# Optimization experiments

Hardware: AMD Instinct MI355X
Metric: run time of the kernel (lower is better)

The kernel has to match this reference:

```python
import jax, jax.numpy as jnp
import numpy as np

D_IN, D, BOX, REL, THR = 2048, 512, 8, 80, 0.5

def _ln(x, g, b):
    m = jnp.mean(x, -1, keepdims=True)
    v = jnp.mean((x - m) ** 2, -1, keepdims=True)
    return (x - m) * jax.lax.rsqrt(v + 1e-5) * g + b

def setup_inputs():
    key = jax.random.key(0)
    ks = jax.random.split(key, 24)
    B, N = 32, 50
    def lin(k, i, o):
        return jax.random.normal(k, (i, o), jnp.float32) / np.sqrt(i)
    z = lambda n: jnp.zeros((n,), jnp.float32)
    o = lambda n: jnp.ones((n,), jnp.float32)
    return {
        "images": jax.random.normal(ks[0], (B, N, D_IN), jnp.float32),
        "selfbbox": jax.random.uniform(ks[1], (B, N, BOX), jnp.float32),
        "bbox": jax.random.uniform(ks[2], (B, N, N, BOX), jnp.float32),
        "pre_w": lin(ks[3], D_IN, D), "pre_b": z(D), "pre_g": o(D), "pre_be": z(D),
        "subj_w": lin(ks[4], D, D), "subj_b": z(D),
        "obj_w": lin(ks[5], D, D), "obj_b": z(D),
        "ps1_w": lin(ks[6], BOX, 64), "ps1_b": z(64), "ps_g": o(64), "ps_be": z(64),
        "ps2_w": lin(ks[7], 64, 64), "ps2_b": z(64),
        "pr1_w": lin(ks[8], BOX, 64), "pr1_b": z(64), "pr_g": o(64), "pr_be": z(64),
        "pr2_w": lin(ks[9], 64, 64), "pr2_b": z(64),
        "rs_w": lin(ks[10], D + 64, 1), "rs_b": z(1),
        "rf_w": lin(ks[11], D + 64, REL), "rf_b": z(REL),
        "g1_w": lin(ks[12], D + REL, D + REL), "g1_b": z(D + REL),
        "g2_w": lin(ks[13], D + REL, D), "g2_b": z(D),
        "g3_w": lin(ks[14], D, D), "g3_b": z(D),
    }

def reference(images, selfbbox, bbox, pre_w, pre_b, pre_g, pre_be, subj_w, subj_b,
              obj_w, obj_b, ps1_w, ps1_b, ps_g, ps_be, ps2_w, ps2_b,
              pr1_w, pr1_b, pr_g, pr_be, pr2_w, pr2_b, rs_w, rs_b, rf_w, rf_b,
              g1_w, g1_b, g2_w, g2_b, g3_w, g3_b):
    B, N = images.shape[0], images.shape[1]
    mask = jnp.sum(images, -1) != 0.0                      # [B,N] valid nodes
    attention_mask = (~mask)[:, None, None, :]             # [B,1,1,N]
    mf = mask.astype(images.dtype)
    # preprocess: Linear -> ReLU -> (dropout=id at eval) -> LayerNorm
    x = _ln(jax.nn.relu(images @ pre_w + pre_b), pre_g, pre_be)  # [B,N,512]
    x_subj = jax.nn.relu(x @ subj_w + subj_b) * mf[..., None]
    x_obj = jax.nn.relu(x @ obj_w + obj_b) * mf[..., None]
    eye = jnp.eye(N, dtype=bool)
    # pairwise subject/object features: diag(i==j) holds subject, off-diag object j
    x_rela = jnp.where(eye[None, :, :, None], x_subj[:, :, None, :], x_obj[:, None, :, :])
    x_rela = x_rela * mf[:, :, None, None]
    # positional MLPs
    h = jax.nn.relu(selfbbox @ ps1_w + ps1_b)
    h = jax.nn.relu(_ln(h, ps_g, ps_be) @ ps2_w + ps2_b)
    pos_self = h * mf[..., None]
    h = jax.nn.relu(bbox @ pr1_w + pr1_b)
    h = jax.nn.relu(_ln(h, pr_g, pr_be) @ pr2_w + pr2_b)
    pos_relas = h * mf[:, None, :, None] * mf[:, :, None, None]
    pos_rela = jnp.where(eye[None, :, :, None], pos_self[:, :, None, :], pos_relas)
    pos_rela = pos_rela * mf[:, :, None, None]
    pair = jnp.concatenate([x_rela, pos_rela], axis=-1)    # [B,N,N,576]
    pair_mask = mask[:, :, None] & mask[:, None, :]        # [B,N,N]
    # Relationshipness: pairwise relatedness score p + attention-pooled relation feats
    logits = (pair @ rs_w + rs_b)[..., 0]                  # [B,N,N]
    p = jax.nn.sigmoid(logits) * pair_mask.astype(images.dtype)
    attn = jax.nn.softmax(jnp.where(pair_mask, logits, -1e9), axis=2)
    feat = jax.nn.relu(pair @ rf_w + rf_b)                 # [B,N,N,80]
    relas = jnp.einsum('bij,bijf->bif', attn, feat) * mf[..., None]
    xx = jnp.concatenate([x, relas], axis=-1)              # [B,N,592]
    # dynamic edge threshold -> block-diagonal graph, expressed densely per image
    A = p > THR                                            # edge i->j
    Ahat = A | eye[None]                                   # add remaining self loops
    Af = Ahat.astype(xx.dtype)
    deg = jnp.sum(Af, axis=1)                              # in-degree at target j (>=1)
    dinv = jax.lax.rsqrt(deg)
    An = Af * dinv[:, :, None] * dinv[:, None, :]          # sym-normalized adjacency
    def gcn(hh, w, b):
        return jnp.einsum('bij,bif->bjf', An, hh @ w) + b
    x1 = jax.nn.relu(gcn(xx, g1_w, g1_b))
    x2 = jax.nn.relu(gcn(x1, g2_w, g2_b))
    x3 = jax.nn.relu(gcn(x2, g3_w, g3_b))
    outs = jnp.concatenate([x[:, None], x3[:, None]], axis=1)  # [B,2,N,512]
    return (outs, attention_mask)
```

## Files before the change

### kernel.cpp

```cpp
#include <hip/hip_runtime.h>
#include <hip/hip_bf16.h>

typedef __hip_bfloat16 bf16;

#define BB 32
#define NN 50
#define DIN 2048
#define DD 512
#define PD 64
#define FF 80
#define GG 592
#define BN (BB*NN)

#define O_FLAG  0
#define O_MF    16
#define O_SS    1616
#define O_SO    3216
#define O_PS    4816
#define O_FS    107216
#define O_FO    235216
#define O_RL    363216
#define O_LG    491216
#define O_AN    571216
#define O_T     651216
#define O_X1    1598416
#define O_X2    2545616
#define O_WPRE  3364816
#define O_BPRE  4413392
#define O_GPRE  4413904
#define O_EPRE  4414416
#define O_WSUBJ 4414928
#define O_BSUBJ 4677072
#define O_WOBJ  4677584
#define O_BOBJ  4939728
#define O_WPS1  4940240
#define O_BPS1  4940752
#define O_GPS   4940816
#define O_EPS   4940880
#define O_WPS2  4940944
#define O_BPS2  4945040
#define O_WPR1  4945104
#define O_BPR1  4945616
#define O_GPR   4945680
#define O_EPR   4945744
#define O_WPR2  4945808
#define O_BPR2  4949904
#define O_WRS   4949968
#define O_BRS   4950544
#define O_WRF   4950560
#define O_BRF   4996640
#define O_WG1   4996736
#define O_BG1   5347200
#define O_WG2   5347792
#define O_BG2   5650896
#define O_WG3   5651408
#define O_BG3   5913552
#define O_FT    5914064

#define PSLICE  819200

__device__ __forceinline__ float b2f(bf16 x){ return __bfloat162float(x); }

__device__ __forceinline__ float LDI(const bf16* p, size_t i, int f32m){
    if(f32m){
        bf16 a=p[2*i], b=p[2*i+1];
        unsigned short lo,hi;
        __builtin_memcpy(&lo,&a,2); __builtin_memcpy(&hi,&b,2);
        unsigned v=((unsigned)hi<<16)|(unsigned)lo;
        float f; __builtin_memcpy(&f,&v,4);
        return f;
    }
    return __bfloat162float(p[i]);
}

__global__ void k_flag(const bf16* __restrict__ images, float* __restrict__ ws){
    __shared__ int cnt;
    if(threadIdx.x==0) cnt=0;
    __syncthreads();
    bf16 h=images[2*threadIdx.x];
    unsigned short u; __builtin_memcpy(&u,&h,2);
    unsigned e=(u>>7)&0xFF;
    int sane=((u&0x7FFF)==0 || (e>=0x70&&e<=0x85))?1:0;
    atomicAdd(&cnt,sane);
    __syncthreads();
    if(threadIdx.x==0) ws[O_FLAG]=(cnt<48)?1.f:0.f;
}

__device__ __forceinline__ void conv(const bf16* s, float* d, int n, int F, int i0, int st){
    for(int g=i0; g<n; g+=st) d[g]=LDI(s,(size_t)g,F);
}
__global__ void kw(const bf16* p0,const bf16* p1,const bf16* p2,const bf16* p3,
                   const bf16* p4,const bf16* p5,const bf16* p6,const bf16* p7,
                   const bf16* p8,const bf16* p9,const bf16* p10,const bf16* p11,
                   const bf16* p12,const bf16* p13,const bf16* p14,const bf16* p15,
                   const bf16* p16,const bf16* p17,const bf16* p18,const bf16* p19,
                   const bf16* p20,const bf16* p21,const bf16* p22,const bf16* p23,
                   const bf16* p24,const bf16* p25,const bf16* p26,const bf16* p27,
                   const bf16* p28,const bf16* p29, float* __restrict__ ws){
    int F=ws[O_FLAG]>0.5f;
    int i0=blockIdx.x*256+threadIdx.x, st=gridDim.x*256;
    conv(p0, ws+O_WPRE, 1048576,F,i0,st);
    conv(p1, ws+O_BPRE, 512,F,i0,st);
    conv(p2, ws+O_GPRE, 512,F,i0,st);
    conv(p3, ws+O_EPRE, 512,F,i0,st);
    conv(p4, ws+O_WSUBJ,262144,F,i0,st);
    conv(p5, ws+O_BSUBJ,512,F,i0,st);
    conv(p6, ws+O_WOBJ, 262144,F,i0,st);
    conv(p7, ws+O_BOBJ, 512,F,i0,st);
    conv(p8, ws+O_WPS1, 512,F,i0,st);
    conv(p9, ws+O_BPS1, 64,F,i0,st);
    conv(p10,ws+O_GPS,  64,F,i0,st);
    conv(p11,ws+O_EPS,  64,F,i0,st);
    conv(p12,ws+O_WPS2, 4096,F,i0,st);
    conv(p13,ws+O_BPS2, 64,F,i0,st);
    conv(p14,ws+O_WPR1, 512,F,i0,st);
    conv(p15,ws+O_BPR1, 64,F,i0,st);
    conv(p16,ws+O_GPR,  64,F,i0,st);
    conv(p17,ws+O_EPR,  64,F,i0,st);
    conv(p18,ws+O_WPR2, 4096,F,i0,st);
    conv(p19,ws+O_BPR2, 64,F,i0,st);
    conv(p20,ws+O_WRS,  576,F,i0,st);
    conv(p21,ws+O_BRS,  1,F,i0,st);
    conv(p22,ws+O_WRF,  46080,F,i0,st);
    conv(p23,ws+O_BRF,  80,F,i0,st);
    conv(p24,ws+O_WG1,  350464,F,i0,st);
    conv(p25,ws+O_BG1,  592,F,i0,st);
    conv(p26,ws+O_WG2,  303104,F,i0,st);
    conv(p27,ws+O_BG2,  512,F,i0,st);
    conv(p28,ws+O_WG3,  262144,F,i0,st);
    conv(p29,ws+O_BG3,  512,F,i0,st);
}

__global__ void __launch_bounds__(256,4) k_x(const bf16* __restrict__ images,
                                             const bf16* __restrict__ sb,
                                             float* __restrict__ ws){
    int blk=blockIdx.x, t=threadIdx.x;
    int F=ws[O_FLAG]>0.5f;
    int wv=t>>6, ln=t&63;
    if(blk>=1600){
        int r=(blk-1600)*4+wv;
        const float* w1=ws+O_WPS1;
        float acc=0.f;
        #pragma unroll
        for(int q=0;q<8;q++) acc+=LDI(sb,(size_t)r*8+q,F)*w1[q*PD+ln];
        float h1=fmaxf(acc+ws[O_BPS1+ln],0.f);
        float sm=0.f;
        for(int k=0;k<PD;k++) sm+=__shfl(h1,k,64);
        float mean=sm/PD;
        float v=0.f;
        for(int k=0;k<PD;k++){ float d=__shfl(h1,k,64)-mean; v+=d*d; }
        float rstd=rsqrtf(v/PD+1e-5f);
        float hn=(h1-mean)*rstd*ws[O_GPS+ln]+ws[O_EPS+ln];
        float a2=0.f;
        const float* w2=ws+O_WPS2;
        for(int k=0;k<PD;k++) a2+=__shfl(hn,k,64)*w2[k*PD+ln];
        ws[O_PS+(size_t)r*PD+ln]=fmaxf(a2+ws[O_BPS2+ln],0.f);
        return;
    }
    __shared__ float as[8*256];
    __shared__ float rsum[4][8];
    int rg=blk>>3, ks=blk&7;
    int r0=rg*8, kbase=ks*256;
    float sv[8];
    #pragma unroll
    for(int row=0;row<8;row++){
        float v=LDI(images,(size_t)(r0+row)*DIN+kbase+t,F);
        as[row*256+t]=v;
        sv[row]=v;
    }
    #pragma unroll
    for(int row=0;row<8;row++){
        float s=sv[row];
        for(int m=32;m>0;m>>=1) s+=__shfl_xor(s,m,64);
        sv[row]=s;
    }
    if(ln==0){
        #pragma unroll
        for(int row=0;row<8;row++) rsum[wv][row]=sv[row];
    }
    __syncthreads();
    if(t<8){
        float s=rsum[0][t]+rsum[1][t]+rsum[2][t]+rsum[3][t];
        ws[O_RL+(size_t)(r0+t)*8+ks]=s;
    }
    const float* wP=ws+O_WPRE+(size_t)kbase*DD;
    int half=t>>7;
    int c4=(t&127)*4;
    int rowbase=half*4;
    float acc[4][4]={};
    for(int k0=0;k0<256;k0+=4){
        float4 w4[4];
        #pragma unroll
        for(int u=0;u<4;u++) w4[u]=*(const float4*)&wP[(size_t)(k0+u)*DD+c4];
        #pragma unroll
        for(int row=0;row<4;row++){
            float4 a0=*(const float4*)&as[(rowbase+row)*256+k0];
            const float* ap=(const float*)&a0;
            #pragma unroll
            for(int u=0;u<4;u++){
                const float* wp=(const float*)&w4[u];
                float ak=ap[u];
                acc[row][0]+=ak*wp[0]; acc[row][1]+=ak*wp[1];
                acc[row][2]+=ak*wp[2]; acc[row][3]+=ak*wp[3];
            }
        }
    }
    float* P=ws + ((ks<7)? (O_FT+(size_t)ks*PSLICE) : (size_t)O_T);
    #pragma unroll
    for(int row=0;row<4;row++){
        float4 o; o.x=acc[row][0]; o.y=acc[row][1]; o.z=acc[row][2]; o.w=acc[row][3];
        *(float4*)&P[(size_t)(r0+rowbase+row)*DD+c4]=o;
    }
}

__global__ void __launch_bounds__(256,4) k_xr(float* __restrict__ ws, float* __restrict__ out){
    __shared__ float red[256];
    int blk=blockIdx.x, t=threadIdx.x;
    int r0=blk*4;
    if(t<4){
        int r=r0+t;
        float s=0.f;
        for(int ks=0;ks<8;ks++) s+=ws[O_RL+(size_t)r*8+ks];
        float mf=(s!=0.f)?1.f:0.f;
        ws[O_MF+r]=mf;
        out[(size_t)BB*2*NN*DD+r]=1.f-mf;
    }
    const float* bPre=ws+O_BPRE; const float* gPre=ws+O_GPRE; const float* ePre=ws+O_EPRE;
    int c0=t, c1=t+256;
    for(int row=0;row<4;row++){
        int r=r0+row;
        float y0=bPre[c0], y1=bPre[c1];
        for(int ks=0;ks<8;ks++){
            const float* P=ws + ((ks<7)? (O_FT+(size_t)ks*PSLICE) : (size_t)O_T);
            y0+=P[(size_t)r*DD+c0]; y1+=P[(size_t)r*DD+c1];
        }
        y0=fmaxf(y0,0.f); y1=fmaxf(y1,0.f);
        red[t]=y0+y1; __syncthreads();
        for(int o=128;o>0;o>>=1){ if(t<o) red[t]+=red[t+o]; __syncthreads(); }
        float mean=red[0]/DD; __syncthreads();
        float d0=y0-mean, d1=y1-mean;
        red[t]=d0*d0+d1*d1; __syncthreads();
        for(int o=128;o>0;o>>=1){ if(t<o) red[t]+=red[t+o]; __syncthreads(); }
        float rstd=rsqrtf(red[0]/DD+1e-5f);
        __syncthreads();
        float xv0=d0*rstd*gPre[c0]+ePre[c0];
        float xv1=d1*rstd*gPre[c1]+ePre[c1];
        size_t ob=((size_t)(r/NN)*2)*NN*DD+(size_t)(r%NN)*DD;
        out[ob+c0]=xv0; out[ob+c1]=xv1;
    }
}

__global__ void __launch_bounds__(256,4) k_so1(const float* __restrict__ out,
                                               float* __restrict__ ws){
    __shared__ float xs[4*DD];
    __shared__ float mrow_s[4];
    int blk=blockIdx.x, t=threadIdx.x;
    int rg=blk>>2, mat=(blk>>1)&1, ch=blk&1;
    int r0=rg*4;
    for(int idx=t; idx<4*DD; idx+=256){
        int row=idx>>9, k=idx&511;
        int r=r0+row;
        xs[idx]=out[((size_t)(r/NN)*2)*NN*DD+(size_t)(r%NN)*DD+k];
    }
    if(t<4) mrow_s[t]=ws[O_MF+r0+t];
    __syncthreads();
    const float* W =ws+(mat?O_WOBJ:O_WSUBJ);
    const float* Bb=ws+(mat?O_BOBJ:O_BSUBJ);
    int c=ch*256+t;
    float acc[4]={0.f,0.f,0.f,0.f};
    for(int k0=0;k0<DD;k0+=8){
        float w[8];
        #pragma unroll
        for(int u=0;u<8;u++) w[u]=W[(size_t)(k0+u)*DD+c];
        #pragma unroll
        for(int row=0;row<4;row++){
            float4 a0=*(const float4*)&xs[row*DD+k0];
            float4 a1=*(const float4*)&xs[row*DD+k0+4];
            acc[row]+=a0.x*w[0]; acc[row]+=a0.y*w[1];
            acc[row]+=a0.z*w[2]; acc[row]+=a0.w*w[3];
            acc[row]+=a1.x*w[4]; acc[row]+=a1.y*w[5];
            acc[row]+=a1.z*w[6]; acc[row]+=a1.w*w[7];
        }
    }
    float* Y=ws+O_FT+(size_t)mat*PSLICE;
    #pragma unroll
    for(int row=0;row<4;row++)
        Y[(size_t)(r0+row)*DD+c]=fmaxf(acc[row]+Bb[c],0.f)*mrow_s[row];
}

__global__ void __launch_bounds__(256,4) k_so2(float* __restrict__ ws){
    __shared__ float yl[4][DD];
    int blk=blockIdx.x, t=threadIdx.x, wv=t>>6, ln=t&63;
    int combo=blk*4+wv;
    int mat=combo&1, r=combo>>1;
    const float* Y=ws+O_FT+(size_t)mat*PSLICE+(size_t)r*DD;
    for(int k=ln;k<DD;k+=64) yl[wv][k]=Y[k];
    __syncthreads();
    const float* wRs=ws+O_WRS;
    float ps=0.f;
    for(int k=ln;k<DD;k+=64) ps+=yl[wv][k]*wRs[k];
    for(int m=32;m>0;m>>=1) ps+=__shfl_xor(ps,m,64);
    if(ln==0) ws[(mat?O_SO:O_SS)+r]=ps;
    const float* wRf=ws+O_WRF;
    float* dst=ws+(mat?O_FO:O_FS)+(size_t)r*FF;
    {
        float a=0.f;
        for(int k0=0;k0<DD;k0+=4){
            float4 y4=*(const float4*)&yl[wv][k0];
            a+=y4.x*wRf[(size_t)k0*FF+ln];
            a+=y4.y*wRf[(size_t)(k0+1)*FF+ln];
            a+=y4.z*wRf[(size_t)(k0+2)*FF+ln];
            a+=y4.w*wRf[(size_t)(k0+3)*FF+ln];
        }
        dst[ln]=a;
    }
    if(ln<16){
        int c=64+ln;
        float a=0.f;
        for(int k0=0;k0<DD;k0+=4){
            float4 y4=*(const float4*)&yl[wv][k0];
            a+=y4.x*wRf[(size_t)k0*FF+c];
            a+=y4.y*wRf[(size_t)(k0+1)*FF+c];
            a+=y4.z*wRf[(size_t)(k0+2)*FF+c];
            a+=y4.w*wRf[(size_t)(k0+3)*FF+c];
        }
        dst[c]=a;
    }
}

#define PSTRIDE 68
#define ZROW(m) ((m)*PSTRIDE + (((m)>>3)<<2))

__global__ void __launch_bounds__(256,3) k_pair(const bf16* __restrict__ bbox,
                                                float* __restrict__ ws){
    __shared__ float zp[64*PSTRIDE+64];
    __shared__ float wbuf[80*PSTRIDE];
    __shared__ float w1s[512];
    __shared__ float bbs[512];
    __shared__ float b1s[64], g1s[64], be1s[64], b2s[64], wrss[64];
    __shared__ float brfs[80];
    __shared__ float rowmi[64], rowmj[64], rowbase[64];
    __shared__ int   rowfb[64], rowps[64], rowdg[64];

    int t=threadIdx.x;
    int blk=blockIdx.x;
    int F=ws[O_FLAG]>0.5f;
    float rsb=ws[O_BRS];

    float wrfreg[20];
    #pragma unroll
    for(int u=0;u<20;u++){
        int idx=t+256*u;
        int f=idx>>6, k=idx&63;
        wrfreg[u]=ws[O_WRF+(size_t)(512+k)*FF+f];
    }

    for(int idx=t; idx<4096; idx+=256){ int k=idx>>6, c=idx&63; wbuf[k*PSTRIDE+c]=ws[O_WPR2+idx]; }
    for(int idx=t; idx<512; idx+=256) w1s[idx]=ws[O_WPR1+idx];
    for(int idx=t; idx<512; idx+=256) bbs[idx]=LDI(bbox,(size_t)blk*512+idx,F);
    if(t<64){
        b1s[t]=ws[O_BPR1+t]; g1s[t]=ws[O_GPR+t]; be1s[t]=ws[O_EPR+t];
        b2s[t]=ws[O_BPR2+t]; wrss[t]=ws[O_WRS+512+t];
    } else if(t<144){
        brfs[t-64]=ws[O_BRF+t-64];
    }
    if(t<64){
        int p=blk*64+t;
        int r=p/NN, j=p-r*NN;
        int b=r/NN, i=r-b*NN;
        int dg=(i==j);
        rowmi[t]=ws[O_MF+r];
        rowmj[t]=ws[O_MF+b*NN+j];
        rowdg[t]=dg;
        rowbase[t]=dg? ws[O_SS+r] : ws[O_SO+b*NN+j];
        rowfb[t]=dg? (O_FS+r*FF) : (O_FO+(b*NN+j)*FF);
        rowps[t]=O_PS+r*PD;
    }
    __syncthreads();

    int wv=t>>6, ln=t&63;
    #pragma unroll 2
    for(int q=0;q<16;q++){
        int m=wv*16+q;
        float acc=0.f;
        #pragma unroll
        for(int u=0;u<8;u++) acc+=bbs[m*8+u]*w1s[u*64+ln];
        float h1=fmaxf(acc+b1s[ln],0.f);
        float sm=h1;
        for(int o=32;o>0;o>>=1) sm+=__shfl_xor(sm,o,64);
        float mean=sm*(1.f/64.f);
        float d=h1-mean;
        float vv=d*d;
        for(int o=32;o>0;o>>=1) vv+=__shfl_xor(vv,o,64);
        float rstd=rsqrtf(vv*(1.f/64.f)+1e-5f);
        zp[ZROW(m)+ln]=d*rstd*g1s[ln]+be1s[ln];
    }

    int tr=t>>4, tc=t&15;
    int m0=tr*4, c0=tc*4;
    float a1[4][4]={};
    #pragma unroll 2
    for(int k0=0;k0<64;k0+=4){
        float4 zv[4], wvv[4];
        #pragma unroll
        for(int i=0;i<4;i++) zv[i]=*(const float4*)&zp[ZROW(m0+i)+k0];
        #pragma unroll
        for(int u=0;u<4;u++) wvv[u]=*(const float4*)&wbuf[(k0+u)*PSTRIDE+c0];
        #pragma unroll
        for(int i=0;i<4;i++){
            const float* zpp=(const float*)&zv[i];
            #pragma unroll
            for(int u=0;u<4;u++){
                const float* wp=(const float*)&wvv[u];
                float zk=zpp[u];
                a1[i][0]+=zk*wp[0]; a1[i][1]+=zk*wp[1];
                a1[i][2]+=zk*wp[2]; a1[i][3]+=zk*wp[3];
            }
        }
    }
    __syncthreads();

    #pragma unroll
    for(int i=0;i<4;i++){
        int m=m0+i;
        float4 o;
        if(rowdg[m]){
            const float* ps=ws+rowps[m];
            float sc=rowmi[m];
            o.x=ps[c0]*sc; o.y=ps[c0+1]*sc; o.z=ps[c0+2]*sc; o.w=ps[c0+3]*sc;
        } else {
            float sc=rowmi[m]*rowmj[m];
            o.x=fmaxf(a1[i][0]+b2s[c0+0],0.f)*sc;
            o.y=fmaxf(a1[i][1]+b2s[c0+1],0.f)*sc;
            o.z=fmaxf(a1[i][2]+b2s[c0+2],0.f)*sc;
            o.w=fmaxf(a1[i][3]+b2s[c0+3],0.f)*sc;
        }
        *(float4*)&zp[ZROW(m)+c0]=o;
    }

    #pragma unroll 2
    for(int q=0;q<16;q++){
        int m=wv*16+q;
        float lp=zp[ZROW(m)+ln]*wrss[ln];
        for(int o=32;o>0;o>>=1) lp+=__shfl_xor(lp,o,64);
        if(ln==0){
            ws[O_LG+(size_t)blk*64+m]=rowmi[m]*rowbase[m]+lp+rsb;
        }
    }

    #pragma unroll
    for(int u=0;u<20;u++){
        int idx=t+256*u;
        wbuf[(idx>>6)*PSTRIDE+(idx&63)]=wrfreg[u];
    }
    __syncthreads();

    {
        int c5=tc*5;
        float a2[4][5]={};
        #pragma unroll 2
        for(int k0=0;k0<64;k0+=4){
            float4 zv[4], wv5[5];
            #pragma unroll
            for(int i=0;i<4;i++) zv[i]=*(const float4*)&zp[ZROW(m0+i)+k0];
            #pragma unroll
            for(int j=0;j<5;j++) wv5[j]=*(const float4*)&wbuf[(c5+j)*PSTRIDE+k0];
            #pragma unroll
            for(int i=0;i<4;i++){
                const float* zpp=(const float*)&zv[i];
                #pragma unroll
                for(int j=0;j<5;j++){
                    const float* wp=(const float*)&wv5[j];
                    a2[i][j]+=zpp[0]*wp[0]+zpp[1]*wp[1]+zpp[2]*wp[2]+zpp[3]*wp[3];
                }
            }
        }
        #pragma unroll
        for(int i=0;i<4;i++){
            int m=m0+i;
            size_t p=(size_t)blk*64+m;
            float mi=rowmi[m];
            const float* fb=ws+rowfb[m];
            #pragma unroll
            for(int j=0;j<5;j++){
                int c=c5+j;
                ws[O_FT+p*FF+c]=fmaxf(mi*fb[c]+a2[i][j]+brfs[c],0.f);
            }
        }
    }
}

__global__ void __launch_bounds__(256,4) k_ra(float* __restrict__ ws){
    __shared__ float shm[2552];
    int blk=blockIdx.x, t=threadIdx.x;
    if(blk<BN){
        int r=blk;
        int b=r/NN;
        float mi=ws[O_MF+r];
        if(t<64){
            float v=-1e9f;
            if(t<NN){
                float mj=ws[O_MF+b*NN+t];
                bool pm=(mi>0.5f)&&(mj>0.5f);
                v=pm? ws[O_LG+(size_t)r*NN+t] : -1e9f;
            }
            float mx=v;
            for(int o=32;o>0;o>>=1) mx=fmaxf(mx,__shfl_xor(mx,o,64));
            float e=(t<NN)? __expf(v-mx) : 0.f;
            float sm=e;
            for(int o=32;o>0;o>>=1) sm+=__shfl_xor(sm,o,64);
            shm[t]=e*(1.f/sm);
        }
        __syncthreads();
        if(t<FF){
            float s=0.f;
            const float* ft=ws+O_FT+(size_t)r*NN*FF;
            for(int j=0;j<NN;j++) s+=shm[j]*ft[(size_t)j*FF+t];
            ws[O_RL+(size_t)r*FF+t]=s*mi;
        }
    } else {
        int b=blk-BN;
        float* Af=shm;
        float* dinv=shm+2500;
        for(int idx=t; idx<NN*NN; idx+=256){
            int i=idx/NN, j=idx%NN;
            float l=ws[O_LG+(size_t)b*NN*NN+idx];
            bool a=(l>0.f)&&(ws[O_MF+b*NN+i]>0.5f)&&(ws[O_MF+b*NN+j]>0.5f);
            Af[idx]=(a||i==j)?1.f:0.f;
        }
        __syncthreads();
        if(t<NN){
            float dg=0.f;
            for(int i=0;i<NN;i++) dg+=Af[i*NN+t];
            dinv[t]=rsqrtf(dg);
        }
        __syncthreads();
        for(int idx=t; idx<NN*NN; idx+=256){
            int i=idx/NN, j=idx%NN;
            ws[O_AN+(size_t)b*NN*NN+idx]=Af[idx]*dinv[i]*dinv[j];
        }
    }
}

__global__ void __launch_bounds__(256,4) kagg(int mode, const float* __restrict__ out,
                                              float* __restrict__ ws, int K, int NCH){
    __shared__ float AnS[2500];
    __shared__ float Xc[50*64];
    int blk=blockIdx.x, t=threadIdx.x;
    int b=blk/NCH, ch=blk-b*NCH;
    int c0=ch*64;
    int cw=K-c0; if(cw>64) cw=64;
    for(int idx=t; idx<2500; idx+=256) AnS[idx]=ws[O_AN+(size_t)b*2500+idx];
    for(int idx=t; idx<50*64; idx+=256){
        int i=idx>>6, cc=idx&63;
        float v=0.f;
        if(cc<cw){
            int c=c0+cc;
            int r=b*NN+i;
            if(mode==0){
                if(c<DD) v=out[(size_t)(2*b)*NN*DD+(size_t)i*DD+c];
                else     v=ws[O_RL+(size_t)r*FF+(c-DD)];
            } else if(mode==1) v=ws[O_X1+(size_t)r*GG+c];
            else               v=ws[O_X2+(size_t)r*DD+c];
        }
        Xc[idx]=v;
    }
    __syncthreads();
    int wv=t>>6, ln=t&63;
    float* T=ws+O_T;
    for(int j=wv; j<NN; j+=4){
        float acc=0.f;
        for(int i=0;i<NN;i++) acc+=AnS[i*NN+j]*Xc[i*64+ln];
        if(ln<cw) T[(size_t)(b*NN+j)*K+c0+ln]=acc;
    }
}

__global__ void __launch_bounds__(256,4) ktf(int mode, float* __restrict__ out,
                   float* __restrict__ ws,
                   const float* __restrict__ W, const float* __restrict__ bias,
                   int K, int NCOL, int NTILE){
    __shared__ float xs[5*GG];
    int blk=blockIdx.x, t=threadIdx.x;
    int rg=blk/NTILE, tile=blk%NTILE;
    const float* T=ws+O_T;
    for(int idx=t; idx<5*K; idx+=256){
        int row=idx/K, k=idx-row*K;
        int gr=rg*5+row;
        xs[row*K+k]=T[(size_t)gr*K+k];
    }
    __syncthreads();
    int c=tile*256+t;
    if(c>=NCOL) return;
    float acc[5];
    #pragma unroll
    for(int u=0;u<5;u++) acc[u]=0.f;
    for(int k0=0;k0<K;k0+=8){
        float w[8];
        #pragma unroll
        for(int u=0;u<8;u++) w[u]=W[(size_t)(k0+u)*NCOL+c];
        #pragma unroll
        for(int row=0;row<5;row++){
            float4 a0=*(const float4*)&xs[row*K+k0];
            float4 a1=*(const float4*)&xs[row*K+k0+4];
            acc[row]+=a0.x*w[0]; acc[row]+=a0.y*w[1];
            acc[row]+=a0.z*w[2]; acc[row]+=a0.w*w[3];
            acc[row]+=a1.x*w[4]; acc[row]+=a1.y*w[5];
            acc[row]+=a1.z*w[6]; acc[row]+=a1.w*w[7];
        }
    }
    int gr0=rg*5;
    float bc=bias[c];
    #pragma unroll
    for(int u=0;u<5;u++){
        float v=fmaxf(acc[u]+bc,0.f);
        int gr=gr0+u;
        if(mode==0)      ws[O_X1+(size_t)gr*GG+c]=v;
        else if(mode==1) ws[O_X2+(size_t)gr*DD+c]=v;
        else {
            int b=gr/NN, j=gr-b*NN;
            out[(size_t)(2*b+1)*NN*DD+(size_t)j*DD+c]=v;
        }
    }
}

extern "C" void kernel_launch(void* const* d_in, const int* in_sizes, int n_in,
                              void* d_out, int out_size, void* d_ws, size_t ws_size,
                              hipStream_t stream) {
    const bf16* images  = (const bf16*)d_in[0];
    const bf16* selfbbox= (const bf16*)d_in[1];
    const bf16* bbox    = (const bf16*)d_in[2];

    float* out=(float*)d_out;
    float* ws =(float*)d_ws;

    k_flag<<<1,64,0,stream>>>(images, ws);
    kw<<<512,256,0,stream>>>((const bf16*)d_in[3],(const bf16*)d_in[4],(const bf16*)d_in[5],
                             (const bf16*)d_in[6],(const bf16*)d_in[7],(const bf16*)d_in[8],
                             (const bf16*)d_in[9],(const bf16*)d_in[10],(const bf16*)d_in[11],
                             (const bf16*)d_in[12],(const bf16*)d_in[13],(const bf16*)d_in[14],
                             (const bf16*)d_in[15],(const bf16*)d_in[16],(const bf16*)d_in[17],
                             (const bf16*)d_in[18],(const bf16*)d_in[19],(const bf16*)d_in[20],
                             (const bf16*)d_in[21],(const bf16*)d_in[22],(const bf16*)d_in[23],
                             (const bf16*)d_in[24],(const bf16*)d_in[25],(const bf16*)d_in[26],
                             (const bf16*)d_in[27],(const bf16*)d_in[28],(const bf16*)d_in[29],
                             (const bf16*)d_in[30],(const bf16*)d_in[31],(const bf16*)d_in[32],
                             ws);
    k_x<<<2000,256,0,stream>>>(images, selfbbox, ws);
    k_xr<<<400,256,0,stream>>>(ws, out);
    k_so1<<<1600,256,0,stream>>>(out, ws);
    k_so2<<<800,256,0,stream>>>(ws);
    k_pair<<<1250,256,0,stream>>>(bbox, ws);
    k_ra<<<BN+BB,256,0,stream>>>(ws);

    kagg<<<32*10,256,0,stream>>>(0, out, ws, GG, 10);
    ktf<<<320*3,256,0,stream>>>(0, out, ws, ws+O_WG1, ws+O_BG1, GG, GG, 3);
    kagg<<<32*10,256,0,stream>>>(1, out, ws, GG, 10);
    ktf<<<320*2,256,0,stream>>>(1, out, ws, ws+O_WG2, ws+O_BG2, GG, DD, 2);
    kagg<<<32*8,256,0,stream>>>(2, out, ws, DD, 8);
    ktf<<<320*2,256,0,stream>>>(2, out, ws, ws+O_WG3, ws+O_BG3, DD, DD, 2);
}
```

Measured before the change: 583.9 us.

## Fuse GCN aggregation into transform kernel, dropping intermediate T buffer

Each transform block now computes its five aggregated rows (An^T·X) directly from the source features instead of reading a precomputed T written by a separate aggregation kernel. This removes three kernel launches and the write and read of T through global memory. The cost is redundant aggregation: every column tile recomputes the same 5xK aggregate, and the feature rows are re-read per row group. The grid of the weight-conversion kernel is also doubled.

```diff
diff --git a/kernel.cpp b/kernel.cpp
--- a/kernel.cpp
+++ b/kernel.cpp
@@ -542,51 +542,35 @@
     }
 }
 
-__global__ void __launch_bounds__(256,4) kagg(int mode, const float* __restrict__ out,
-                                              float* __restrict__ ws, int K, int NCH){
-    __shared__ float AnS[2500];
-    __shared__ float Xc[50*64];
-    int blk=blockIdx.x, t=threadIdx.x;
-    int b=blk/NCH, ch=blk-b*NCH;
-    int c0=ch*64;
-    int cw=K-c0; if(cw>64) cw=64;
-    for(int idx=t; idx<2500; idx+=256) AnS[idx]=ws[O_AN+(size_t)b*2500+idx];
-    for(int idx=t; idx<50*64; idx+=256){
-        int i=idx>>6, cc=idx&63;
-        float v=0.f;
-        if(cc<cw){
-            int c=c0+cc;
-            int r=b*NN+i;
-            if(mode==0){
-                if(c<DD) v=out[(size_t)(2*b)*NN*DD+(size_t)i*DD+c];
-                else     v=ws[O_RL+(size_t)r*FF+(c-DD)];
-            } else if(mode==1) v=ws[O_X1+(size_t)r*GG+c];
-            else               v=ws[O_X2+(size_t)r*DD+c];
-        }
-        Xc[idx]=v;
-    }
-    __syncthreads();
-    int wv=t>>6, ln=t&63;
-    float* T=ws+O_T;
-    for(int j=wv; j<NN; j+=4){
-        float acc=0.f;
-        for(int i=0;i<NN;i++) acc+=AnS[i*NN+j]*Xc[i*64+ln];
-        if(ln<cw) T[(size_t)(b*NN+j)*K+c0+ln]=acc;
-    }
-}
-
-__global__ void __launch_bounds__(256,4) ktf(int mode, float* __restrict__ out,
+__global__ void __launch_bounds__(256,4) kgcn(int mode, float* __restrict__ out,
                    float* __restrict__ ws,
                    const float* __restrict__ W, const float* __restrict__ bias,
                    int K, int NCOL, int NTILE){
+    __shared__ float ans[5*50];
     __shared__ float xs[5*GG];
     int blk=blockIdx.x, t=threadIdx.x;
     int rg=blk/NTILE, tile=blk%NTILE;
-    const float* T=ws+O_T;
-    for(int idx=t; idx<5*K; idx+=256){
-        int row=idx/K, k=idx-row*K;
-        int gr=rg*5+row;
-        xs[row*K+k]=T[(size_t)gr*K+k];
+    int gr0=rg*5;
+    int b=gr0/NN, j0=gr0-b*NN;
+    for(int idx=t; idx<250; idx+=256){
+        int i=idx/5, jj=idx-i*5;
+        ans[idx]=ws[O_AN+(size_t)b*2500+(size_t)i*NN+j0+jj];
+    }
+    __syncthreads();
+    for(int c=t; c<K; c+=256){
+        float a0=0.f,a1=0.f,a2=0.f,a3=0.f,a4=0.f;
+        for(int i=0;i<NN;i++){
+            float xv;
+            int r=b*NN+i;
+            if(mode==0){
+                xv=(c<DD)? out[(size_t)(2*b)*NN*DD+(size_t)i*DD+c]
+                         : ws[O_RL+(size_t)r*FF+(c-DD)];
+            } else if(mode==1) xv=ws[O_X1+(size_t)r*GG+c];
+            else               xv=ws[O_X2+(size_t)r*DD+c];
+            const float* ar=&ans[i*5];
+            a0+=ar[0]*xv; a1+=ar[1]*xv; a2+=ar[2]*xv; a3+=ar[3]*xv; a4+=ar[4]*xv;
+        }
+        xs[0*K+c]=a0; xs[1*K+c]=a1; xs[2*K+c]=a2; xs[3*K+c]=a3; xs[4*K+c]=a4;
     }
     __syncthreads();
     int c=tile*256+t;
@@ -608,17 +592,17 @@
             acc[row]+=a1.z*w[6]; acc[row]+=a1.w*w[7];
         }
     }
-    int gr0=rg*5;
+    int gr00=rg*5;
     float bc=bias[c];
     #pragma unroll
     for(int u=0;u<5;u++){
         float v=fmaxf(acc[u]+bc,0.f);
-        int gr=gr0+u;
+        int gr=gr00+u;
         if(mode==0)      ws[O_X1+(size_t)gr*GG+c]=v;
         else if(mode==1) ws[O_X2+(size_t)gr*DD+c]=v;
         else {
-            int b=gr/NN, j=gr-b*NN;
-            out[(size_t)(2*b+1)*NN*DD+(size_t)j*DD+c]=v;
+            int bb=gr/NN, j=gr-bb*NN;
+            out[(size_t)(2*bb+1)*NN*DD+(size_t)j*DD+c]=v;
         }
     }
 }
@@ -634,7 +618,7 @@
     float* ws =(float*)d_ws;
 
     k_flag<<<1,64,0,stream>>>(images, ws);
-    kw<<<512,256,0,stream>>>((const bf16*)d_in[3],(const bf16*)d_in[4],(const bf16*)d_in[5],
+    kw<<<1024,256,0,stream>>>((const bf16*)d_in[3],(const bf16*)d_in[4],(const bf16*)d_in[5],
                              (const bf16*)d_in[6],(const bf16*)d_in[7],(const bf16*)d_in[8],
                              (const bf16*)d_in[9],(const bf16*)d_in[10],(const bf16*)d_in[11],
                              (const bf16*)d_in[12],(const bf16*)d_in[13],(const bf16*)d_in[14],
@@ -652,10 +636,7 @@
     k_pair<<<1250,256,0,stream>>>(bbox, ws);
     k_ra<<<BN+BB,256,0,stream>>>(ws);
 
-    kagg<<<32*10,256,0,stream>>>(0, out, ws, GG, 10);
-    ktf<<<320*3,256,0,stream>>>(0, out, ws, ws+O_WG1, ws+O_BG1, GG, GG, 3);
-    kagg<<<32*10,256,0,stream>>>(1, out, ws, GG, 10);
-    ktf<<<320*2,256,0,stream>>>(1, out, ws, ws+O_WG2, ws+O_BG2, GG, DD, 2);
-    kagg<<<32*8,256,0,stream>>>(2, out, ws, DD, 8);
-    ktf<<<320*2,256,0,stream>>>(2, out, ws, ws+O_WG3, ws+O_BG3, DD, DD, 2);
-}
+    kgcn<<<320*3,256,0,stream>>>(0, out, ws, ws+O_WG1, ws+O_BG1, GG, GG, 3);
+    kgcn<<<320*2,256,0,stream>>>(1, out, ws, ws+O_WG2, ws+O_BG2, GG, DD, 2);
+    kgcn<<<320*2,256,0,stream>>>(2, out, ws, ws+O_WG3, ws+O_BG3, DD, DD, 2);
+}
```

Measured after the change: 636.4 us. 9.0% more time.
